# Kernel tuning notes

Hardware: AMD Instinct MI355X
Metric: run time of the kernel (lower is better)

## Reference

```python
import jax, jax.numpy as jnp
import numpy as np

E, H, F = 8, 1024, 2048   # experts, hidden, ffn
B, S = 1, 1024
JITTER = 0.01             # router_jitter_noise


def setup_inputs() -> dict:
    key = jax.random.key(0)
    ks = jax.random.split(key, 5)
    return {
        "hidden_states": jax.random.normal(ks[0], (B, S, H), jnp.float32),
        "gate_w": jax.random.normal(ks[1], (E, H), jnp.float32) * 0.02,
        "w1": jax.random.normal(ks[2], (E, F, H), jnp.float32) * 0.02,
        "w2": jax.random.normal(ks[3], (E, H, F), jnp.float32) * 0.02,
        "w3": jax.random.normal(ks[4], (E, F, H), jnp.float32) * 0.02,
    }


def _sparsemixer_eval(scores, jitter_eps):
    # scores: [T, E]. Inference path of sparsemixer (training=False).
    T = scores.shape[0]
    rows = jnp.arange(T)
    # top-1
    max1 = jnp.max(scores, axis=-1, keepdims=True)
    sel1 = jnp.argmax(scores, axis=-1)
    factor1 = jnp.maximum(jnp.abs(scores), max1)          # scores.abs().clamp(min=max1)
    mask1 = (max1 - scores) / factor1 > 2.0 * jitter_eps
    gates1 = jax.nn.softmax(jnp.where(mask1, -jnp.inf, scores), axis=-1)
    mult1 = gates1[rows, sel1]
    # top-2: mask out the top-1 expert
    masked_scores = scores.at[rows, sel1].set(-jnp.inf)
    max2 = jnp.max(masked_scores, axis=-1, keepdims=True)
    sel2 = jnp.argmax(masked_scores, axis=-1)
    factor2 = jnp.maximum(jnp.abs(scores), max2)
    mask2 = (max2 - scores) / factor2 > 2.0 * jitter_eps
    gates2 = jax.nn.softmax(jnp.where(mask2, -jnp.inf, masked_scores), axis=-1)
    mult2 = gates2[rows, sel2]
    multiplier = jnp.stack([mult1, mult2], axis=-1)       # [T, 2]
    selected = jnp.stack([sel1, sel2], axis=-1)           # [T, 2]
    return multiplier, selected


def reference(hidden_states, gate_w, w1, w2, w3):
    b, s, h = hidden_states.shape
    x = hidden_states.reshape(-1, h)                      # [T, H]
    router_logits = x @ gate_w.T                          # [T, E]
    mult, sel = _sparsemixer_eval(router_logits, JITTER)
    n_exp = gate_w.shape[0]
    # combined routing weight per (token, expert): sum of top-k multipliers
    weight = jnp.sum(mult[..., None] * jax.nn.one_hot(sel, n_exp, dtype=x.dtype), axis=1)  # [T, E]
    # dense masked dispatch: evaluate every expert, combine with routing weights
    h1 = jnp.einsum('th,efh->etf', x, w1)                 # [E, T, F]
    h3 = jnp.einsum('th,efh->etf', x, w3)
    inter = jax.nn.silu(h1) * h3
    out_e = jnp.einsum('etf,ehf->eth', inter, w2)         # [E, T, H]
    final = jnp.einsum('eth,te->th', out_e, weight)       # [T, H]
    return final.reshape(b, s, h), router_logits
```

## Files before the change

### kernel.cpp

```cpp
#include <hip/hip_runtime.h>
#include <hip/hip_bf16.h>
#include <math.h>


#define T_TOK 1024
#define H_DIM 1024
#define F_DIM 2048
#define N_EXP 8
#define JIT 0.01f

#define BK  64
#define LDK 68
#define NK1 (H_DIM / BK)
#define NK2 (F_DIM / BK)
#define MT1_MAX 16
#define MT2_MAX 24

typedef __bf16 bf16_t;
typedef __bf16 bf16x8 __attribute__((ext_vector_type(8)));
typedef __bf16 bf16x4 __attribute__((ext_vector_type(4)));
typedef float f32x4 __attribute__((ext_vector_type(4)));

__device__ inline bf16x4 cvt4(float4 v) {
    bf16x4 r;
    r[0] = (bf16_t)v.x; r[1] = (bf16_t)v.y; r[2] = (bf16_t)v.z; r[3] = (bf16_t)v.w;
    return r;
}

#define WS_CNT   0
#define WS_BASE  64
#define WS_TOK   128
#define WS_WGT   (128 + 32768)
#define WS_SLOT  (WS_WGT + 32768)
#define WS_INTER 131072
#define WS_ACC   (131072 + 8388608)

__global__ __launch_bounds__(256) void router_k(
    const float* __restrict__ x, const float* __restrict__ gw,
    float* __restrict__ logits_out,
    int* __restrict__ cnt, int* __restrict__ tok,
    float* __restrict__ wgt, int* __restrict__ slot)
{
    int t = blockIdx.x;
    int tid = threadIdx.x;
    __shared__ float sm[N_EXP][256];

    float acc[N_EXP];
#pragma unroll
    for (int e = 0; e < N_EXP; e++) acc[e] = 0.f;
#pragma unroll
    for (int j = 0; j < H_DIM / 256; j++) {
        int h = tid + j * 256;
        float xv = x[t * H_DIM + h];
#pragma unroll
        for (int e = 0; e < N_EXP; e++) acc[e] += xv * gw[e * H_DIM + h];
    }
#pragma unroll
    for (int e = 0; e < N_EXP; e++) sm[e][tid] = acc[e];
    __syncthreads();
    for (int s = 128; s > 0; s >>= 1) {
        if (tid < s) {
#pragma unroll
            for (int e = 0; e < N_EXP; e++) sm[e][tid] += sm[e][tid + s];
        }
        __syncthreads();
    }
    if (tid == 0) {
        float s[N_EXP];
#pragma unroll
        for (int e = 0; e < N_EXP; e++) {
            s[e] = sm[e][0];
            logits_out[t * N_EXP + e] = s[e];
        }
        float max1 = -INFINITY; int sel1 = 0;
        for (int e = 0; e < N_EXP; e++) if (s[e] > max1) { max1 = s[e]; sel1 = e; }
        float denom1 = 0.f;
        for (int e = 0; e < N_EXP; e++) {
            float factor = fmaxf(fabsf(s[e]), max1);
            bool m = ((max1 - s[e]) / factor) > (2.0f * JIT);
            if (!m) denom1 += expf(s[e] - max1);
        }
        float mult1 = 1.0f / denom1;
        float max2 = -INFINITY; int sel2 = 0;
        for (int e = 0; e < N_EXP; e++)
            if (e != sel1 && s[e] > max2) { max2 = s[e]; sel2 = e; }
        float denom2 = 0.f;
        for (int e = 0; e < N_EXP; e++) {
            if (e == sel1) continue;
            float factor = fmaxf(fabsf(s[e]), max2);
            bool m = ((max2 - s[e]) / factor) > (2.0f * JIT);
            if (!m) denom2 += expf(s[e] - max2);
        }
        float mult2 = 1.0f / denom2;

        int p1 = atomicAdd(&cnt[sel1], 1);
        tok[sel1 * T_TOK + p1] = t; wgt[sel1 * T_TOK + p1] = mult1; slot[sel1 * T_TOK + p1] = 0;
        int p2 = atomicAdd(&cnt[sel2], 1);
        tok[sel2 * T_TOK + p2] = t; wgt[sel2 * T_TOK + p2] = mult2; slot[sel2 * T_TOK + p2] = 1;
    }
}

__global__ void prefix_k(const int* __restrict__ cnt, int* __restrict__ base)
{
    if (threadIdx.x == 0 && blockIdx.x == 0) {
        int a = 0;
        for (int e = 0; e < N_EXP; e++) { base[e] = a; a += cnt[e]; }
    }
}

__global__ __launch_bounds__(512, 2) void gemm1_k(
    const float* __restrict__ x,
    const float* __restrict__ w1,
    const float* __restrict__ w3,
    const int* __restrict__ cnt, const int* __restrict__ base,
    const int* __restrict__ tok,
    bf16_t* __restrict__ inter)
{
    int mt = blockIdx.x >> 5;
    int nt = blockIdx.x & 31;
    int e = 0, m0 = 0, found = 0, accb = 0;
#pragma unroll
    for (int ee = 0; ee < N_EXP; ee++) {
        int b = (cnt[ee] + 255) >> 8;
        if (!found && mt < accb + b) { e = ee; m0 = (mt - accb) << 8; found = 1; }
        accb += b;
    }
    if (!found) return;
    int cntE = cnt[e];
    int n0 = nt * 64;
    int tid = threadIdx.x;
    int lane = tid & 63, quad = lane >> 4, l16 = lane & 15;
    int wave = tid >> 6;
    int wm = wave >> 1, wn = wave & 1;

    __shared__ __align__(16) bf16_t Al[2][256 * LDK];
    __shared__ __align__(16) bf16_t B1l[2][64 * LDK];
    __shared__ __align__(16) bf16_t B3l[2][64 * LDK];
    __shared__ int tokL[256];

    if (tid < 256) {
        int r = m0 + tid;
        tokL[tid] = tok[e * T_TOK + (r < cntE ? r : cntE - 1)];
    }
    __syncthreads();

    int rA[8], kA[8];
    const float* aP[8];
#pragma unroll
    for (int i = 0; i < 8; i++) {
        int c = tid + i * 512;
        rA[i] = c >> 4; kA[i] = c & 15;
        aP[i] = x + (size_t)tokL[rA[i]] * H_DIM + kA[i] * 4;
    }
    int rB[2], kB[2];
    const float *b1P[2], *b3P[2];
    const float* w1e = w1 + (size_t)e * F_DIM * H_DIM + (size_t)n0 * H_DIM;
    const float* w3e = w3 + (size_t)e * F_DIM * H_DIM + (size_t)n0 * H_DIM;
#pragma unroll
    for (int i = 0; i < 2; i++) {
        int c = tid + i * 512;
        rB[i] = c >> 4; kB[i] = c & 15;
        b1P[i] = w1e + (size_t)rB[i] * H_DIM + kB[i] * 4;
        b3P[i] = w3e + (size_t)rB[i] * H_DIM + kB[i] * 4;
    }

    f32x4 acc1[4][2], acc3[4][2];
#pragma unroll
    for (int fi = 0; fi < 4; fi++)
#pragma unroll
        for (int fj = 0; fj < 2; fj++) {
            acc1[fi][fj] = f32x4{0.f, 0.f, 0.f, 0.f};
            acc3[fi][fj] = f32x4{0.f, 0.f, 0.f, 0.f};
        }

    float4 pA[2][8], p1[2][2], p3[2][2];
#pragma unroll
    for (int i = 0; i < 8; i++) pA[0][i] = *(const float4*)(aP[i]);
#pragma unroll
    for (int i = 0; i < 2; i++) { p1[0][i] = *(const float4*)(b1P[i]); p3[0][i] = *(const float4*)(b3P[i]); }

#pragma unroll 2
    for (int kk = 0; kk < NK1; kk++) {
        const int cur = kk & 1, nxt = cur ^ 1;
        if (kk + 1 < NK1) {
            const int k0 = (kk + 1) * BK;
#pragma unroll
            for (int i = 0; i < 8; i++) pA[nxt][i] = *(const float4*)(aP[i] + k0);
#pragma unroll
            for (int i = 0; i < 2; i++) {
                p1[nxt][i] = *(const float4*)(b1P[i] + k0);
                p3[nxt][i] = *(const float4*)(b3P[i] + k0);
            }
        }
        __builtin_amdgcn_sched_barrier(0);
#pragma unroll
        for (int i = 0; i < 8; i++)
            *(bf16x4*)&Al[cur][rA[i] * LDK + kA[i] * 4] = cvt4(pA[cur][i]);
#pragma unroll
        for (int i = 0; i < 2; i++) {
            *(bf16x4*)&B1l[cur][rB[i] * LDK + kB[i] * 4] = cvt4(p1[cur][i]);
            *(bf16x4*)&B3l[cur][rB[i] * LDK + kB[i] * 4] = cvt4(p3[cur][i]);
        }
        asm volatile("s_waitcnt lgkmcnt(0)" ::: "memory");
        __builtin_amdgcn_s_barrier();
#pragma unroll
        for (int s = 0; s < 2; s++) {
            int ko = s * 32 + quad * 8;
            bf16x8 af[4], b1f[2], b3f[2];
#pragma unroll
            for (int fi = 0; fi < 4; fi++)
                af[fi] = *(const bf16x8*)&Al[cur][(wm * 64 + fi * 16 + l16) * LDK + ko];
#pragma unroll
            for (int fj = 0; fj < 2; fj++) {
                b1f[fj] = *(const bf16x8*)&B1l[cur][(wn * 32 + fj * 16 + l16) * LDK + ko];
                b3f[fj] = *(const bf16x8*)&B3l[cur][(wn * 32 + fj * 16 + l16) * LDK + ko];
            }
#pragma unroll
            for (int fi = 0; fi < 4; fi++)
#pragma unroll
                for (int fj = 0; fj < 2; fj++) {
                    acc1[fi][fj] = __builtin_amdgcn_mfma_f32_16x16x32_bf16(af[fi], b1f[fj], acc1[fi][fj], 0, 0, 0);
                    acc3[fi][fj] = __builtin_amdgcn_mfma_f32_16x16x32_bf16(af[fi], b3f[fj], acc3[fi][fj], 0, 0, 0);
                }
        }
    }

    int rowBase = base[e];
#pragma unroll
    for (int fi = 0; fi < 4; fi++)
#pragma unroll
        for (int fj = 0; fj < 2; fj++) {
            int ff = n0 + wn * 32 + fj * 16 + l16;
#pragma unroll
            for (int r = 0; r < 4; r++) {
                int mm = m0 + wm * 64 + fi * 16 + quad * 4 + r;
                if (mm < cntE) {
                    float h1 = acc1[fi][fj][r], h3 = acc3[fi][fj][r];
                    float v = (h1 / (1.f + expf(-h1))) * h3;
                    inter[(size_t)(rowBase + mm) * F_DIM + ff] = (bf16_t)v;
                }
            }
        }
}

__global__ __launch_bounds__(512, 2) void gemm2_k(
    const bf16_t* __restrict__ inter,
    const float* __restrict__ w2,
    const int* __restrict__ cnt, const int* __restrict__ base,
    const int* __restrict__ tok,
    const float* __restrict__ wgt, const int* __restrict__ slot,
    float* __restrict__ accOut)
{
    int mt = blockIdx.x >> 4;
    int nt = blockIdx.x & 15;
    int e = 0, m0 = 0, found = 0, accb = 0;
#pragma unroll
    for (int ee = 0; ee < N_EXP; ee++) {
        int b = (cnt[ee] + 127) >> 7;
        if (!found && mt < accb + b) { e = ee; m0 = (mt - accb) << 7; found = 1; }
        accb += b;
    }
    if (!found) return;
    int cntE = cnt[e];
    int n0 = nt * 64;
    int tid = threadIdx.x;
    int lane = tid & 63, quad = lane >> 4, l16 = lane & 15;
    int wave = tid >> 6;
    int wm = wave >> 1, wn = wave & 1;
    int rowBase = base[e];

    __shared__ __align__(16) bf16_t Al[2][128 * LDK];
    __shared__ __align__(16) bf16_t Bl[2][64 * LDK];

    int rA[2], kA[2];
    const bf16_t* aP[2];
#pragma unroll
    for (int i = 0; i < 2; i++) {
        int c = tid + i * 512;
        rA[i] = c >> 3; kA[i] = c & 7;
        int row = m0 + rA[i]; if (row >= cntE) row = cntE - 1;
        aP[i] = inter + (size_t)(rowBase + row) * F_DIM + kA[i] * 8;
    }
    int rB[2], kB[2];
    const float* bP[2];
    const float* w2e = w2 + (size_t)e * H_DIM * F_DIM + (size_t)n0 * F_DIM;
#pragma unroll
    for (int i = 0; i < 2; i++) {
        int c = tid + i * 512;
        rB[i] = c >> 4; kB[i] = c & 15;
        bP[i] = w2e + (size_t)rB[i] * F_DIM + kB[i] * 4;
    }

    f32x4 acc[2][2];
#pragma unroll
    for (int fi = 0; fi < 2; fi++)
#pragma unroll
        for (int fj = 0; fj < 2; fj++) acc[fi][fj] = f32x4{0.f, 0.f, 0.f, 0.f};

    bf16x8 pa[2][2];
    float4 pb[2][2];
#pragma unroll
    for (int i = 0; i < 2; i++) { pa[0][i] = *(const bf16x8*)(aP[i]); pb[0][i] = *(const float4*)(bP[i]); }

#pragma unroll 2
    for (int kk = 0; kk < NK2; kk++) {
        const int cur = kk & 1, nxt = cur ^ 1;
        if (kk + 1 < NK2) {
            const int k0 = (kk + 1) * BK;
#pragma unroll
            for (int i = 0; i < 2; i++) {
                pa[nxt][i] = *(const bf16x8*)(aP[i] + k0);
                pb[nxt][i] = *(const float4*)(bP[i] + k0);
            }
        }
        __builtin_amdgcn_sched_barrier(0);
#pragma unroll
        for (int i = 0; i < 2; i++) {
            *(bf16x8*)&Al[cur][rA[i] * LDK + kA[i] * 8] = pa[cur][i];
            *(bf16x4*)&Bl[cur][rB[i] * LDK + kB[i] * 4] = cvt4(pb[cur][i]);
        }
        asm volatile("s_waitcnt lgkmcnt(0)" ::: "memory");
        __builtin_amdgcn_s_barrier();
#pragma unroll
        for (int s = 0; s < 2; s++) {
            int ko = s * 32 + quad * 8;
            bf16x8 af[2], bfr[2];
#pragma unroll
            for (int fi = 0; fi < 2; fi++)
                af[fi] = *(const bf16x8*)&Al[cur][(wm * 32 + fi * 16 + l16) * LDK + ko];
#pragma unroll
            for (int fj = 0; fj < 2; fj++)
                bfr[fj] = *(const bf16x8*)&Bl[cur][(wn * 32 + fj * 16 + l16) * LDK + ko];
#pragma unroll
            for (int fi = 0; fi < 2; fi++)
#pragma unroll
                for (int fj = 0; fj < 2; fj++)
                    acc[fi][fj] = __builtin_amdgcn_mfma_f32_16x16x32_bf16(af[fi], bfr[fj], acc[fi][fj], 0, 0, 0);
        }
    }

#pragma unroll
    for (int fi = 0; fi < 2; fi++)
#pragma unroll
        for (int r = 0; r < 4; r++) {
            int mm = m0 + wm * 32 + fi * 16 + quad * 4 + r;
            if (mm < cntE) {
                int t = tok[e * T_TOK + mm];
                float wv = wgt[e * T_TOK + mm];
                int sl = slot[e * T_TOK + mm];
                float* dst = accOut + (size_t)sl * T_TOK * H_DIM + (size_t)t * H_DIM;
#pragma unroll
                for (int fj = 0; fj < 2; fj++)
                    dst[n0 + wn * 32 + fj * 16 + l16] = acc[fi][fj][r] * wv;
            }
        }
}

__global__ __launch_bounds__(256) void combine_k(const float* __restrict__ acc,
                                                 float* __restrict__ out)
{
    int i = blockIdx.x * 256 + threadIdx.x;
    const float4* a0 = (const float4*)acc;
    const float4* a1 = (const float4*)(acc + (size_t)T_TOK * H_DIM);
    float4 v0 = a0[i];
    float4 v1 = a1[i];
    float4 r;
    r.x = v0.x + v1.x; r.y = v0.y + v1.y; r.z = v0.z + v1.z; r.w = v0.w + v1.w;
    ((float4*)out)[i] = r;
}

extern "C" void kernel_launch(void* const* d_in, const int* in_sizes, int n_in,
                              void* d_out, int out_size, void* d_ws, size_t ws_size,
                              hipStream_t stream) {
    const float* x  = (const float*)d_in[0];
    const float* gw = (const float*)d_in[1];
    const float* w1 = (const float*)d_in[2];
    const float* w2 = (const float*)d_in[3];
    const float* w3 = (const float*)d_in[4];
    float* out = (float*)d_out;
    float* logits_out = out + (size_t)T_TOK * H_DIM;

    char* ws = (char*)d_ws;
    int*    cnt   = (int*)(ws + WS_CNT);
    int*    basep = (int*)(ws + WS_BASE);
    int*    tok   = (int*)(ws + WS_TOK);
    float*  wgt   = (float*)(ws + WS_WGT);
    int*    slot  = (int*)(ws + WS_SLOT);
    bf16_t* inter = (bf16_t*)(ws + WS_INTER);
    float*  accO  = (float*)(ws + WS_ACC);

    hipMemsetAsync(cnt, 0, 64, stream);
    router_k<<<T_TOK, 256, 0, stream>>>(x, gw, logits_out, cnt, tok, wgt, slot);
    prefix_k<<<1, 64, 0, stream>>>(cnt, basep);
    gemm1_k<<<dim3(MT1_MAX * 32), 512, 0, stream>>>(x, w1, w3, cnt, basep, tok, inter);
    gemm2_k<<<dim3(MT2_MAX * 16), 512, 0, stream>>>(inter, w2, cnt, basep, tok, wgt, slot, accO);
    combine_k<<<(T_TOK * H_DIM / 4) / 256, 256, 0, stream>>>(accO, out);
}
```

Baseline: 321.6 us.

## Rewrite router as wave-per-token and retile expert GEMMs to 256-thread blocks

The router now gives each token to one wavefront, using float4 loads and shuffle reductions in place of a shared-memory tree with many barriers, and packs four tokens per block. The gemm1 row tile drops from 256 to 128 tokens, so less padding is wasted on small per-expert counts. Both GEMMs move to 256 threads, where each wave owns 32 rows across the full 64-column tile, and gemm2 raises its occupancy hint. Register double-buffering of global loads is replaced by a single prefetch set issued after a __syncthreads, which may expose more load latency.

```diff
diff --git a/kernel.cpp b/kernel.cpp
--- a/kernel.cpp
+++ b/kernel.cpp
@@ -13,8 +13,7 @@
 #define LDK 68
 #define NK1 (H_DIM / BK)
 #define NK2 (F_DIM / BK)
-#define MT1_MAX 16
-#define MT2_MAX 24
+#define MT_MAX 24
 
 typedef __bf16 bf16_t;
 typedef __bf16 bf16x8 __attribute__((ext_vector_type(8)));
@@ -41,35 +40,33 @@
     int* __restrict__ cnt, int* __restrict__ tok,
     float* __restrict__ wgt, int* __restrict__ slot)
 {
-    int t = blockIdx.x;
-    int tid = threadIdx.x;
-    __shared__ float sm[N_EXP][256];
+    int wave = threadIdx.x >> 6, lane = threadIdx.x & 63;
+    int t = blockIdx.x * 4 + wave;
+    const float* xr = x + (size_t)t * H_DIM;
+    int h0 = lane * 16;
 
     float acc[N_EXP];
 #pragma unroll
     for (int e = 0; e < N_EXP; e++) acc[e] = 0.f;
 #pragma unroll
-    for (int j = 0; j < H_DIM / 256; j++) {
-        int h = tid + j * 256;
-        float xv = x[t * H_DIM + h];
-#pragma unroll
-        for (int e = 0; e < N_EXP; e++) acc[e] += xv * gw[e * H_DIM + h];
-    }
-#pragma unroll
-    for (int e = 0; e < N_EXP; e++) sm[e][tid] = acc[e];
-    __syncthreads();
-    for (int s = 128; s > 0; s >>= 1) {
-        if (tid < s) {
-#pragma unroll
-            for (int e = 0; e < N_EXP; e++) sm[e][tid] += sm[e][tid + s];
-        }
-        __syncthreads();
-    }
-    if (tid == 0) {
+    for (int j = 0; j < 16; j += 4) {
+        float4 xv = *(const float4*)(xr + h0 + j);
+#pragma unroll
+        for (int e = 0; e < N_EXP; e++) {
+            float4 gv = *(const float4*)(gw + e * H_DIM + h0 + j);
+            acc[e] += xv.x * gv.x + xv.y * gv.y + xv.z * gv.z + xv.w * gv.w;
+        }
+    }
+#pragma unroll
+    for (int m = 32; m > 0; m >>= 1)
+#pragma unroll
+        for (int e = 0; e < N_EXP; e++) acc[e] += __shfl_xor(acc[e], m, 64);
+
+    if (lane == 0) {
         float s[N_EXP];
 #pragma unroll
         for (int e = 0; e < N_EXP; e++) {
-            s[e] = sm[e][0];
+            s[e] = acc[e];
             logits_out[t * N_EXP + e] = s[e];
         }
         float max1 = -INFINITY; int sel1 = 0;
@@ -108,7 +105,7 @@
     }
 }
 
-__global__ __launch_bounds__(512, 2) void gemm1_k(
+__global__ __launch_bounds__(256, 2) void gemm1_k(
     const float* __restrict__ x,
     const float* __restrict__ w1,
     const float* __restrict__ w3,
@@ -121,8 +118,8 @@
     int e = 0, m0 = 0, found = 0, accb = 0;
 #pragma unroll
     for (int ee = 0; ee < N_EXP; ee++) {
-        int b = (cnt[ee] + 255) >> 8;
-        if (!found && mt < accb + b) { e = ee; m0 = (mt - accb) << 8; found = 1; }
+        int b = (cnt[ee] + 127) >> 7;
+        if (!found && mt < accb + b) { e = ee; m0 = (mt - accb) << 7; found = 1; }
         accb += b;
     }
     if (!found) return;
@@ -131,94 +128,91 @@
     int tid = threadIdx.x;
     int lane = tid & 63, quad = lane >> 4, l16 = lane & 15;
     int wave = tid >> 6;
-    int wm = wave >> 1, wn = wave & 1;
-
-    __shared__ __align__(16) bf16_t Al[2][256 * LDK];
+
+    __shared__ __align__(16) bf16_t Al[2][128 * LDK];
     __shared__ __align__(16) bf16_t B1l[2][64 * LDK];
     __shared__ __align__(16) bf16_t B3l[2][64 * LDK];
-    __shared__ int tokL[256];
-
-    if (tid < 256) {
+    __shared__ int tokL[128];
+
+    if (tid < 128) {
         int r = m0 + tid;
         tokL[tid] = tok[e * T_TOK + (r < cntE ? r : cntE - 1)];
     }
     __syncthreads();
 
-    int rA[8], kA[8];
-    const float* aP[8];
+    int rA[8], kA[8], ofsA[8];
 #pragma unroll
     for (int i = 0; i < 8; i++) {
-        int c = tid + i * 512;
+        int c = tid + i * 256;
         rA[i] = c >> 4; kA[i] = c & 15;
-        aP[i] = x + (size_t)tokL[rA[i]] * H_DIM + kA[i] * 4;
-    }
-    int rB[2], kB[2];
-    const float *b1P[2], *b3P[2];
-    const float* w1e = w1 + (size_t)e * F_DIM * H_DIM + (size_t)n0 * H_DIM;
-    const float* w3e = w3 + (size_t)e * F_DIM * H_DIM + (size_t)n0 * H_DIM;
-#pragma unroll
-    for (int i = 0; i < 2; i++) {
-        int c = tid + i * 512;
+        ofsA[i] = tokL[rA[i]] * H_DIM + kA[i] * 4;
+    }
+    int rB[4], kB[4], ofsB[4];
+    const float* w1e = w1 + (size_t)e * F_DIM * H_DIM;
+    const float* w3e = w3 + (size_t)e * F_DIM * H_DIM;
+#pragma unroll
+    for (int i = 0; i < 4; i++) {
+        int c = tid + i * 256;
         rB[i] = c >> 4; kB[i] = c & 15;
-        b1P[i] = w1e + (size_t)rB[i] * H_DIM + kB[i] * 4;
-        b3P[i] = w3e + (size_t)rB[i] * H_DIM + kB[i] * 4;
-    }
-
-    f32x4 acc1[4][2], acc3[4][2];
-#pragma unroll
-    for (int fi = 0; fi < 4; fi++)
-#pragma unroll
-        for (int fj = 0; fj < 2; fj++) {
+        ofsB[i] = (n0 + rB[i]) * H_DIM + kB[i] * 4;
+    }
+
+    f32x4 acc1[2][4], acc3[2][4];
+#pragma unroll
+    for (int fi = 0; fi < 2; fi++)
+#pragma unroll
+        for (int fj = 0; fj < 4; fj++) {
             acc1[fi][fj] = f32x4{0.f, 0.f, 0.f, 0.f};
             acc3[fi][fj] = f32x4{0.f, 0.f, 0.f, 0.f};
         }
 
-    float4 pA[2][8], p1[2][2], p3[2][2];
-#pragma unroll
-    for (int i = 0; i < 8; i++) pA[0][i] = *(const float4*)(aP[i]);
-#pragma unroll
-    for (int i = 0; i < 2; i++) { p1[0][i] = *(const float4*)(b1P[i]); p3[0][i] = *(const float4*)(b3P[i]); }
+    float4 pA[8], p1[4], p3[4];
+#pragma unroll
+    for (int i = 0; i < 8; i++) pA[i] = *(const float4*)(x + ofsA[i]);
+#pragma unroll
+    for (int i = 0; i < 4; i++) {
+        p1[i] = *(const float4*)(w1e + ofsB[i]);
+        p3[i] = *(const float4*)(w3e + ofsB[i]);
+    }
 
 #pragma unroll 2
     for (int kk = 0; kk < NK1; kk++) {
-        const int cur = kk & 1, nxt = cur ^ 1;
+        const int cur = kk & 1;
+#pragma unroll
+        for (int i = 0; i < 8; i++)
+            *(bf16x4*)&Al[cur][rA[i] * LDK + kA[i] * 4] = cvt4(pA[i]);
+#pragma unroll
+        for (int i = 0; i < 4; i++) {
+            *(bf16x4*)&B1l[cur][rB[i] * LDK + kB[i] * 4] = cvt4(p1[i]);
+            *(bf16x4*)&B3l[cur][rB[i] * LDK + kB[i] * 4] = cvt4(p3[i]);
+        }
+        __syncthreads();
         if (kk + 1 < NK1) {
             const int k0 = (kk + 1) * BK;
 #pragma unroll
-            for (int i = 0; i < 8; i++) pA[nxt][i] = *(const float4*)(aP[i] + k0);
-#pragma unroll
-            for (int i = 0; i < 2; i++) {
-                p1[nxt][i] = *(const float4*)(b1P[i] + k0);
-                p3[nxt][i] = *(const float4*)(b3P[i] + k0);
-            }
-        }
-        __builtin_amdgcn_sched_barrier(0);
-#pragma unroll
-        for (int i = 0; i < 8; i++)
-            *(bf16x4*)&Al[cur][rA[i] * LDK + kA[i] * 4] = cvt4(pA[cur][i]);
-#pragma unroll
-        for (int i = 0; i < 2; i++) {
-            *(bf16x4*)&B1l[cur][rB[i] * LDK + kB[i] * 4] = cvt4(p1[cur][i]);
-            *(bf16x4*)&B3l[cur][rB[i] * LDK + kB[i] * 4] = cvt4(p3[cur][i]);
-        }
-        asm volatile("s_waitcnt lgkmcnt(0)" ::: "memory");
-        __builtin_amdgcn_s_barrier();
+            for (int i = 0; i < 8; i++) pA[i] = *(const float4*)(x + ofsA[i] + k0);
+#pragma unroll
+            for (int i = 0; i < 4; i++) {
+                p1[i] = *(const float4*)(w1e + ofsB[i] + k0);
+                p3[i] = *(const float4*)(w3e + ofsB[i] + k0);
+            }
+        }
 #pragma unroll
         for (int s = 0; s < 2; s++) {
             int ko = s * 32 + quad * 8;
-            bf16x8 af[4], b1f[2], b3f[2];
-#pragma unroll
-            for (int fi = 0; fi < 4; fi++)
-                af[fi] = *(const bf16x8*)&Al[cur][(wm * 64 + fi * 16 + l16) * LDK + ko];
-#pragma unroll
-            for (int fj = 0; fj < 2; fj++) {
-                b1f[fj] = *(const bf16x8*)&B1l[cur][(wn * 32 + fj * 16 + l16) * LDK + ko];
-                b3f[fj] = *(const bf16x8*)&B3l[cur][(wn * 32 + fj * 16 + l16) * LDK + ko];
-            }
-#pragma unroll
-            for (int fi = 0; fi < 4; fi++)
-#pragma unroll
-                for (int fj = 0; fj < 2; fj++) {
+            bf16x8 af[2], b1f[4], b3f[4];
+#pragma unroll
+            for (int fi = 0; fi < 2; fi++)
+                af[fi] = *(const bf16x8*)&Al[cur][(wave * 32 + fi * 16 + l16) * LDK + ko];
+#pragma unroll
+            for (int fj = 0; fj < 4; fj++) {
+                b1f[fj] = *(const bf16x8*)&B1l[cur][(fj * 16 + l16) * LDK + ko];
+                b3f[fj] = *(const bf16x8*)&B3l[cur][(fj * 16 + l16) * LDK + ko];
+            }
+#pragma unroll
+            for (int fi = 0; fi < 2; fi++)
+#pragma unroll
+                for (int fj = 0; fj < 4; fj++) {
                     acc1[fi][fj] = __builtin_amdgcn_mfma_f32_16x16x32_bf16(af[fi], b1f[fj], acc1[fi][fj], 0, 0, 0);
                     acc3[fi][fj] = __builtin_amdgcn_mfma_f32_16x16x32_bf16(af[fi], b3f[fj], acc3[fi][fj], 0, 0, 0);
                 }
@@ -227,13 +221,13 @@
 
     int rowBase = base[e];
 #pragma unroll
-    for (int fi = 0; fi < 4; fi++)
-#pragma unroll
-        for (int fj = 0; fj < 2; fj++) {
-            int ff = n0 + wn * 32 + fj * 16 + l16;
+    for (int fi = 0; fi < 2; fi++)
+#pragma unroll
+        for (int fj = 0; fj < 4; fj++) {
+            int ff = n0 + fj * 16 + l16;
 #pragma unroll
             for (int r = 0; r < 4; r++) {
-                int mm = m0 + wm * 64 + fi * 16 + quad * 4 + r;
+                int mm = m0 + wave * 32 + fi * 16 + quad * 4 + r;
                 if (mm < cntE) {
                     float h1 = acc1[fi][fj][r], h3 = acc3[fi][fj][r];
                     float v = (h1 / (1.f + expf(-h1))) * h3;
@@ -243,7 +237,7 @@
         }
 }
 
-__global__ __launch_bounds__(512, 2) void gemm2_k(
+__global__ __launch_bounds__(256, 3) void gemm2_k(
     const bf16_t* __restrict__ inter,
     const float* __restrict__ w2,
     const int* __restrict__ cnt, const int* __restrict__ base,
@@ -266,75 +260,73 @@
     int tid = threadIdx.x;
     int lane = tid & 63, quad = lane >> 4, l16 = lane & 15;
     int wave = tid >> 6;
-    int wm = wave >> 1, wn = wave & 1;
     int rowBase = base[e];
 
     __shared__ __align__(16) bf16_t Al[2][128 * LDK];
     __shared__ __align__(16) bf16_t Bl[2][64 * LDK];
 
-    int rA[2], kA[2];
-    const bf16_t* aP[2];
-#pragma unroll
-    for (int i = 0; i < 2; i++) {
-        int c = tid + i * 512;
+    int rA[4], kA[4], ofsA[4];
+#pragma unroll
+    for (int i = 0; i < 4; i++) {
+        int c = tid + i * 256;
         rA[i] = c >> 3; kA[i] = c & 7;
         int row = m0 + rA[i]; if (row >= cntE) row = cntE - 1;
-        aP[i] = inter + (size_t)(rowBase + row) * F_DIM + kA[i] * 8;
-    }
-    int rB[2], kB[2];
-    const float* bP[2];
-    const float* w2e = w2 + (size_t)e * H_DIM * F_DIM + (size_t)n0 * F_DIM;
-#pragma unroll
-    for (int i = 0; i < 2; i++) {
-        int c = tid + i * 512;
+        ofsA[i] = (rowBase + row) * F_DIM + kA[i] * 8;
+    }
+    int rB[4], kB[4], ofsB[4];
+    const float* w2e = w2 + (size_t)e * H_DIM * F_DIM;
+#pragma unroll
+    for (int i = 0; i < 4; i++) {
+        int c = tid + i * 256;
         rB[i] = c >> 4; kB[i] = c & 15;
-        bP[i] = w2e + (size_t)rB[i] * F_DIM + kB[i] * 4;
-    }
-
-    f32x4 acc[2][2];
+        ofsB[i] = (n0 + rB[i]) * F_DIM + kB[i] * 4;
+    }
+
+    f32x4 acc[2][4];
 #pragma unroll
     for (int fi = 0; fi < 2; fi++)
 #pragma unroll
-        for (int fj = 0; fj < 2; fj++) acc[fi][fj] = f32x4{0.f, 0.f, 0.f, 0.f};
-
-    bf16x8 pa[2][2];
-    float4 pb[2][2];
-#pragma unroll
-    for (int i = 0; i < 2; i++) { pa[0][i] = *(const bf16x8*)(aP[i]); pb[0][i] = *(const float4*)(bP[i]); }
+        for (int fj = 0; fj < 4; fj++) acc[fi][fj] = f32x4{0.f, 0.f, 0.f, 0.f};
+
+    bf16x8 pa[4];
+    float4 pb[4];
+#pragma unroll
+    for (int i = 0; i < 4; i++) {
+        pa[i] = *(const bf16x8*)(inter + ofsA[i]);
+        pb[i] = *(const float4*)(w2e + ofsB[i]);
+    }
 
 #pragma unroll 2
     for (int kk = 0; kk < NK2; kk++) {
-        const int cur = kk & 1, nxt = cur ^ 1;
+        const int cur = kk & 1;
+#pragma unroll
+        for (int i = 0; i < 4; i++) {
+            *(bf16x8*)&Al[cur][rA[i] * LDK + kA[i] * 8] = pa[i];
+            *(bf16x4*)&Bl[cur][rB[i] * LDK + kB[i] * 4] = cvt4(pb[i]);
+        }
+        __syncthreads();
         if (kk + 1 < NK2) {
             const int k0 = (kk + 1) * BK;
 #pragma unroll
-            for (int i = 0; i < 2; i++) {
-                pa[nxt][i] = *(const bf16x8*)(aP[i] + k0);
-                pb[nxt][i] = *(const float4*)(bP[i] + k0);
-            }
-        }
-        __builtin_amdgcn_sched_barrier(0);
-#pragma unroll
-        for (int i = 0; i < 2; i++) {
-            *(bf16x8*)&Al[cur][rA[i] * LDK + kA[i] * 8] = pa[cur][i];
-            *(bf16x4*)&Bl[cur][rB[i] * LDK + kB[i] * 4] = cvt4(pb[cur][i]);
-        }
-        asm volatile("s_waitcnt lgkmcnt(0)" ::: "memory");
-        __builtin_amdgcn_s_barrier();
+            for (int i = 0; i < 4; i++) {
+                pa[i] = *(const bf16x8*)(inter + ofsA[i] + k0);
+                pb[i] = *(const float4*)(w2e + ofsB[i] + k0);
+            }
+        }
 #pragma unroll
         for (int s = 0; s < 2; s++) {
             int ko = s * 32 + quad * 8;
-            bf16x8 af[2], bfr[2];
+            bf16x8 af[2], bfr[4];
 #pragma unroll
             for (int fi = 0; fi < 2; fi++)
-                af[fi] = *(const bf16x8*)&Al[cur][(wm * 32 + fi * 16 + l16) * LDK + ko];
-#pragma unroll
-            for (int fj = 0; fj < 2; fj++)
-                bfr[fj] = *(const bf16x8*)&Bl[cur][(wn * 32 + fj * 16 + l16) * LDK + ko];
+                af[fi] = *(const bf16x8*)&Al[cur][(wave * 32 + fi * 16 + l16) * LDK + ko];
+#pragma unroll
+            for (int fj = 0; fj < 4; fj++)
+                bfr[fj] = *(const bf16x8*)&Bl[cur][(fj * 16 + l16) * LDK + ko];
 #pragma unroll
             for (int fi = 0; fi < 2; fi++)
 #pragma unroll
-                for (int fj = 0; fj < 2; fj++)
+                for (int fj = 0; fj < 4; fj++)
                     acc[fi][fj] = __builtin_amdgcn_mfma_f32_16x16x32_bf16(af[fi], bfr[fj], acc[fi][fj], 0, 0, 0);
         }
     }
@@ -343,15 +335,15 @@
     for (int fi = 0; fi < 2; fi++)
 #pragma unroll
         for (int r = 0; r < 4; r++) {
-            int mm = m0 + wm * 32 + fi * 16 + quad * 4 + r;
+            int mm = m0 + wave * 32 + fi * 16 + quad * 4 + r;
             if (mm < cntE) {
                 int t = tok[e * T_TOK + mm];
                 float wv = wgt[e * T_TOK + mm];
                 int sl = slot[e * T_TOK + mm];
                 float* dst = accOut + (size_t)sl * T_TOK * H_DIM + (size_t)t * H_DIM;
 #pragma unroll
-                for (int fj = 0; fj < 2; fj++)
-                    dst[n0 + wn * 32 + fj * 16 + l16] = acc[fi][fj][r] * wv;
+                for (int fj = 0; fj < 4; fj++)
+                    dst[n0 + fj * 16 + l16] = acc[fi][fj][r] * wv;
             }
         }
 }
@@ -390,9 +382,9 @@
     float*  accO  = (float*)(ws + WS_ACC);
 
     hipMemsetAsync(cnt, 0, 64, stream);
-    router_k<<<T_TOK, 256, 0, stream>>>(x, gw, logits_out, cnt, tok, wgt, slot);
+    router_k<<<T_TOK / 4, 256, 0, stream>>>(x, gw, logits_out, cnt, tok, wgt, slot);
     prefix_k<<<1, 64, 0, stream>>>(cnt, basep);
-    gemm1_k<<<dim3(MT1_MAX * 32), 512, 0, stream>>>(x, w1, w3, cnt, basep, tok, inter);
-    gemm2_k<<<dim3(MT2_MAX * 16), 512, 0, stream>>>(inter, w2, cnt, basep, tok, wgt, slot, accO);
+    gemm1_k<<<dim3(MT_MAX * 32), 256, 0, stream>>>(x, w1, w3, cnt, basep, tok, inter);
+    gemm2_k<<<dim3(MT_MAX * 16), 256, 0, stream>>>(inter, w2, cnt, basep, tok, wgt, slot, accO);
     combine_k<<<(T_TOK * H_DIM / 4) / 256, 256, 0, stream>>>(accO, out);
 }
```

Measured after the change: 314.5 us. 2.2% less time.
